# Optimization experiments

Hardware: AMD Instinct MI355X
Metric: run time of the kernel (lower is better)

## Reference

```python
import jax, jax.numpy as jnp
import numpy as np

NUM_TIME_BLOCKS = 32  # P
B, L, D = 32, 4096, 256


def setup_inputs() -> dict:
    key = jax.random.key(0)
    k1, k2 = jax.random.split(key)
    x = jax.random.normal(k1, (B, L, D), dtype=jnp.float32)
    # normalized timestamps in [0, 1), matching linspace(0, 1.001, P+1) bin edges
    time_steps = jax.random.uniform(k2, (B, L), dtype=jnp.float32)
    return {"x": x, "time_steps": time_steps}


def reference(x, time_steps):
    # Bin edges identical to torch.linspace(0.0, 1.001, P+1)
    blocks = jnp.linspace(0.0, 1.001, NUM_TIME_BLOCKS + 1, dtype=jnp.float32)
    ls = blocks[:-1]  # (P,) left edges (inclusive)
    rs = blocks[1:]   # (P,) right edges (exclusive)
    ts = time_steps[..., None]                      # (B, L, 1)
    # one-hot bucket membership mask, (B, L, P); a token falls in exactly one bin
    mask = ((ts >= ls) & (ts < rs)).astype(x.dtype)
    # sum x over sequence positions within each time bucket -> (B, P, D)
    new_x = jnp.einsum('blp,bld->bpd', mask, x)
    return new_x, time_steps
```

## Files before the change

### kernel.cpp

```cpp
#include <hip/hip_runtime.h>


#define Bk 32
#define Lk 4096
#define Dk 256
#define Pk 32
#define NTH 512
#define NW 8

typedef float v4f __attribute__((ext_vector_type(4)));

__device__ __forceinline__ int bucket_of(float tv) {
    const double step = 1.001 / 32.0;
    int p = (int)(tv * (float)(32.0 / 1.001));
    p = p < 0 ? 0 : (p > 31 ? 31 : p);
    while (p > 0 && tv < (float)((double)p * step)) --p;
    while (p < 31 && tv >= (float)((double)(p + 1) * step)) ++p;
    return p;
}

__global__ __launch_bounds__(NTH, 6) void tc_fused(
        const float* __restrict__ x,
        const float* __restrict__ ts,
        float* __restrict__ out,
        float* __restrict__ ts_out) {
    __shared__ int rows[Lk];
    __shared__ int nrows;
    __shared__ v4f red[NW * 64];

    const int p = blockIdx.x;
    const int b = blockIdx.y;
    const int t = threadIdx.x;
    const int w = t >> 6;
    const int lane = t & 63;
    const int col4 = lane << 2;

    if (t == 0) nrows = 0;
    __syncthreads();

    const float* tsb = ts + (size_t)b * Lk;
#pragma unroll
    for (int k = 0; k < Lk / NTH; ++k) {
        const int l = t + k * NTH;
        const float tv = tsb[l];
        if (p == 0) ts_out[(size_t)b * Lk + l] = tv;
        const bool match = (bucket_of(tv) == p);
        const unsigned long long m = __ballot(match);
        const int nact = __popcll(m);
        int wbase = 0;
        if (lane == 0 && nact) wbase = atomicAdd(&nrows, nact);
        wbase = __shfl(wbase, 0);
        if (match) {
            const int pre = __popcll(m & ((1ull << lane) - 1ull));
            rows[wbase + pre] = l;
        }
    }
    __syncthreads();
    const int cnt = nrows;

    const float* xb = x + (size_t)b * Lk * Dk;
    v4f a0 = 0.f, a1 = 0.f, a2 = 0.f, a3 = 0.f;
    int i = w;
    for (; i + 7 * NW < cnt; i += 8 * NW) {
        int r[8];
#pragma unroll
        for (int j = 0; j < 8; ++j) r[j] = rows[i + j * NW];
        v4f v[8];
#pragma unroll
        for (int j = 0; j < 8; ++j)
            v[j] = __builtin_nontemporal_load(
                (const v4f*)(xb + (size_t)r[j] * Dk + col4));
        a0 += v[0]; a1 += v[1]; a2 += v[2]; a3 += v[3];
        a0 += v[4]; a1 += v[5]; a2 += v[6]; a3 += v[7];
    }
    for (; i < cnt; i += NW) {
        a0 += __builtin_nontemporal_load(
            (const v4f*)(xb + (size_t)rows[i] * Dk + col4));
    }
    a0 += a1; a2 += a3; a0 += a2;

    red[w * 64 + lane] = a0;
    __syncthreads();
    if (w == 0) {
        v4f r = red[lane];
#pragma unroll
        for (int ww = 1; ww < NW; ++ww) r += red[ww * 64 + lane];
        *(v4f*)(out + ((size_t)b * Pk + p) * Dk + col4) = r;
    }
}

extern "C" void kernel_launch(void* const* d_in, const int* in_sizes, int n_in,
                              void* d_out, int out_size, void* d_ws, size_t ws_size,
                              hipStream_t stream) {
    const float* x  = (const float*)d_in[0];
    const float* ts = (const float*)d_in[1];
    float* out = (float*)d_out;
    float* ts_out = out + (size_t)Bk * Pk * Dk;

    dim3 grid(Pk, Bk);
    tc_fused<<<grid, NTH, 0, stream>>>(x, ts, out, ts_out);
}
```

Before: 187.9 us.

## Stream sequence chunks with shared-memory atomic bucket accumulation instead of per-bucket gathers

Each block now takes one chunk of the sequence for one batch entry instead of one time bucket. It classifies that chunk's timestamps, streams x rows contiguously and accumulates them into a per-bucket shared-memory histogram with LDS float atomics. It then adds the partials into the output with global atomics, after zeroing the output with a memset. This replaces the per-bucket scan of all timestamps and the gathered row loads with coalesced streaming. The cost is LDS atomic contention, global atomics, an extra memset, and non-deterministic summation order.

```diff
diff --git a/kernel.cpp b/kernel.cpp
--- a/kernel.cpp
+++ b/kernel.cpp
@@ -5,6 +5,8 @@
 #define Lk 4096
 #define Dk 256
 #define Pk 32
+#define NCHUNK 16
+#define ROWS (Lk / NCHUNK)
 #define NTH 512
 #define NW 8
 
@@ -19,73 +21,56 @@
     return p;
 }
 
-__global__ __launch_bounds__(NTH, 6) void tc_fused(
+__global__ __launch_bounds__(NTH, 4) void tc_stream(
         const float* __restrict__ x,
         const float* __restrict__ ts,
         float* __restrict__ out,
         float* __restrict__ ts_out) {
-    __shared__ int rows[Lk];
-    __shared__ int nrows;
-    __shared__ v4f red[NW * 64];
+    __shared__ float acc[Pk][4][64];
+    __shared__ int pbuf[ROWS];
 
-    const int p = blockIdx.x;
+    const int c = blockIdx.x;
     const int b = blockIdx.y;
     const int t = threadIdx.x;
     const int w = t >> 6;
     const int lane = t & 63;
-    const int col4 = lane << 2;
+    const int base = c * ROWS;
 
-    if (t == 0) nrows = 0;
+    {
+        v4f z = 0.f;
+        v4f* a4 = (v4f*)&acc[0][0][0];
+#pragma unroll
+        for (int i = t; i < Pk * Dk / 4; i += NTH) a4[i] = z;
+    }
+
+    if (t < ROWS) {
+        const size_t li = (size_t)b * Lk + base + t;
+        const float tv = ts[li];
+        ts_out[li] = tv;
+        pbuf[t] = bucket_of(tv);
+    }
     __syncthreads();
 
-    const float* tsb = ts + (size_t)b * Lk;
-#pragma unroll
-    for (int k = 0; k < Lk / NTH; ++k) {
-        const int l = t + k * NTH;
-        const float tv = tsb[l];
-        if (p == 0) ts_out[(size_t)b * Lk + l] = tv;
-        const bool match = (bucket_of(tv) == p);
-        const unsigned long long m = __ballot(match);
-        const int nact = __popcll(m);
-        int wbase = 0;
-        if (lane == 0 && nact) wbase = atomicAdd(&nrows, nact);
-        wbase = __shfl(wbase, 0);
-        if (match) {
-            const int pre = __popcll(m & ((1ull << lane) - 1ull));
-            rows[wbase + pre] = l;
-        }
+    const float* xb = x + ((size_t)b * Lk + base) * Dk;
+#pragma unroll 4
+    for (int r = w; r < ROWS; r += NW) {
+        const int p = pbuf[r];
+        const v4f v = __builtin_nontemporal_load(
+            (const v4f*)(xb + (size_t)r * Dk + (lane << 2)));
+        float* ap = &acc[p][0][lane];
+        unsafeAtomicAdd(ap,       v.x);
+        unsafeAtomicAdd(ap + 64,  v.y);
+        unsafeAtomicAdd(ap + 128, v.z);
+        unsafeAtomicAdd(ap + 192, v.w);
     }
     __syncthreads();
-    const int cnt = nrows;
 
-    const float* xb = x + (size_t)b * Lk * Dk;
-    v4f a0 = 0.f, a1 = 0.f, a2 = 0.f, a3 = 0.f;
-    int i = w;
-    for (; i + 7 * NW < cnt; i += 8 * NW) {
-        int r[8];
+    float* ob = out + (size_t)b * Pk * Dk;
 #pragma unroll
-        for (int j = 0; j < 8; ++j) r[j] = rows[i + j * NW];
-        v4f v[8];
-#pragma unroll
-        for (int j = 0; j < 8; ++j)
-            v[j] = __builtin_nontemporal_load(
-                (const v4f*)(xb + (size_t)r[j] * Dk + col4));
-        a0 += v[0]; a1 += v[1]; a2 += v[2]; a3 += v[3];
-        a0 += v[4]; a1 += v[5]; a2 += v[6]; a3 += v[7];
-    }
-    for (; i < cnt; i += NW) {
-        a0 += __builtin_nontemporal_load(
-            (const v4f*)(xb + (size_t)rows[i] * Dk + col4));
-    }
-    a0 += a1; a2 += a3; a0 += a2;
-
-    red[w * 64 + lane] = a0;
-    __syncthreads();
-    if (w == 0) {
-        v4f r = red[lane];
-#pragma unroll
-        for (int ww = 1; ww < NW; ++ww) r += red[ww * 64 + lane];
-        *(v4f*)(out + ((size_t)b * Pk + p) * Dk + col4) = r;
+    for (int i = t; i < Pk * Dk; i += NTH) {
+        const int p = i >> 8;
+        const int col = i & 255;
+        unsafeAtomicAdd(ob + i, acc[p][col & 3][col >> 2]);
     }
 }
 
@@ -97,6 +82,7 @@
     float* out = (float*)d_out;
     float* ts_out = out + (size_t)Bk * Pk * Dk;
 
-    dim3 grid(Pk, Bk);
-    tc_fused<<<grid, NTH, 0, stream>>>(x, ts, out, ts_out);
+    hipMemsetAsync(out, 0, (size_t)Bk * Pk * Dk * sizeof(float), stream);
+    dim3 grid(NCHUNK, Bk);
+    tc_stream<<<grid, NTH, 0, stream>>>(x, ts, out, ts_out);
 }
```

New measurement: 331.7 us. 1.76x slower.
